# Kernel tuning notes

Measured on AMD Instinct MI355X. Metric: run time of the kernel, lower is better.

Reference implementation:

```python
import jax, jax.numpy as jnp
import numpy as np

D_MODEL = 1024
N_HEAD = 16
D_K = D_MODEL // N_HEAD
FF = 4096
EPS = 1e-5


def _linear(x, W, b):
    # torch nn.Linear: y = x @ W.T + b ; W stored [out, in]
    return jnp.einsum('bnd,od->bno', x, W) + b


def _mha(xq, xkv, Wq, bq, Wk, bk, Wv, bv):
    B, N, D = xq.shape
    M = xkv.shape[1]
    q = _linear(xq, Wq, bq).reshape(B, N, N_HEAD, D_K).transpose(0, 2, 1, 3)
    k = _linear(xkv, Wk, bk).reshape(B, M, N_HEAD, D_K).transpose(0, 2, 1, 3)
    v = _linear(xkv, Wv, bv).reshape(B, M, N_HEAD, D_K).transpose(0, 2, 1, 3)
    scores = jnp.einsum('bhnd,bhmd->bhnm', q, k) / np.sqrt(D_K).astype(np.float32)
    attn = jax.nn.softmax(scores, axis=-1)
    out = jnp.einsum('bhnm,bhmd->bhnd', attn, v)
    return out.transpose(0, 2, 1, 3).reshape(B, N, D)


def _layernorm(x, g, b):
    mu = jnp.mean(x, axis=-1, keepdims=True)
    var = jnp.mean((x - mu) ** 2, axis=-1, keepdims=True)
    return (x - mu) * jax.lax.rsqrt(var + EPS) * g + b


def setup_inputs() -> dict:
    key = jax.random.key(0)
    ks = jax.random.split(key, 24)
    s = 0.02
    d = {
        'x': jax.random.normal(ks[0], (8, 1024, D_MODEL), jnp.float32),
        'memory': jax.random.normal(ks[1], (8, 1024, D_MODEL), jnp.float32),
        'Wq1': jax.random.normal(ks[2], (D_MODEL, D_MODEL), jnp.float32) * s,
        'bq1': jnp.zeros((D_MODEL,), jnp.float32),
        'Wk1': jax.random.normal(ks[3], (D_MODEL, D_MODEL), jnp.float32) * s,
        'bk1': jnp.zeros((D_MODEL,), jnp.float32),
        'Wv1': jax.random.normal(ks[4], (D_MODEL, D_MODEL), jnp.float32) * s,
        'bv1': jnp.zeros((D_MODEL,), jnp.float32),
        'Wq2': jax.random.normal(ks[5], (D_MODEL, D_MODEL), jnp.float32) * s,
        'bq2': jnp.zeros((D_MODEL,), jnp.float32),
        'Wk2': jax.random.normal(ks[6], (D_MODEL, D_MODEL), jnp.float32) * s,
        'bk2': jnp.zeros((D_MODEL,), jnp.float32),
        'Wv2': jax.random.normal(ks[7], (D_MODEL, D_MODEL), jnp.float32) * s,
        'bv2': jnp.zeros((D_MODEL,), jnp.float32),
        'W1': jax.random.normal(ks[8], (FF, D_MODEL), jnp.float32) * s,
        'b1': jnp.zeros((FF,), jnp.float32),
        'W2': jax.random.normal(ks[9], (D_MODEL, FF), jnp.float32) * s,
        'b2': jnp.zeros((D_MODEL,), jnp.float32),
        'g1': jnp.ones((D_MODEL,), jnp.float32),
        'be1': jnp.zeros((D_MODEL,), jnp.float32),
        'g2': jnp.ones((D_MODEL,), jnp.float32),
        'be2': jnp.zeros((D_MODEL,), jnp.float32),
        'g3': jnp.ones((D_MODEL,), jnp.float32),
        'be3': jnp.zeros((D_MODEL,), jnp.float32),
    }
    return d


def reference(x, memory, Wq1, bq1, Wk1, bk1, Wv1, bv1,
              Wq2, bq2, Wk2, bk2, Wv2, bv2,
              W1, b1, W2, b2, g1, be1, g2, be2, g3, be3):
    # Post-LN decoder layer, eval mode (dropout = identity), no masks
    x = _layernorm(x + _mha(x, x, Wq1, bq1, Wk1, bk1, Wv1, bv1), g1, be1)
    x = _layernorm(x + _mha(x, memory, Wq2, bq2, Wk2, bk2, Wv2, bv2), g2, be2)
    h = jnp.einsum('hf,bnf->bnh', W2, jax.nn.relu(_linear(x, W1, b1))) + b2
    x = _layernorm(x + h, g3, be3)
    return x
```

## Files before the change

### kernel.cpp

```cpp
#include <hip/hip_runtime.h>
#include <hip/hip_bf16.h>

typedef __attribute__((ext_vector_type(8))) short bf16x8;
typedef __attribute__((ext_vector_type(4))) float f32x4;

#define DEVI static __device__ __forceinline__

constexpr int DM  = 1024;
constexpr int NH  = 16;
constexpr int FFD = 4096;
constexpr int BB  = 8;
constexpr int SEQ = 1024;
constexpr int TT  = BB * SEQ;

DEVI float bf2f(unsigned short u) {
    union { unsigned u32; float f; } v; v.u32 = ((unsigned)u) << 16; return v.f;
}
DEVI unsigned short f2bf(float f) {
    union { float f; unsigned u; } v; v.f = f;
    unsigned x = v.u;
    return (unsigned short)((x + 0x7fffu + ((x >> 16) & 1u)) >> 16);
}

DEVI void async_ld16(void* lds, const void* g) {
    __builtin_amdgcn_global_load_lds(
        (const __attribute__((address_space(1))) unsigned int*)g,
        (__attribute__((address_space(3))) unsigned int*)lds, 16, 0, 0);
}

__global__ __launch_bounds__(256) void k_cvt(const float* __restrict__ src,
                                             unsigned short* __restrict__ dst, int n) {
    int i = (blockIdx.x * 256 + threadIdx.x) * 4;
    if (i >= n) return;
    float4 v = *reinterpret_cast<const float4*>(src + i);
    ushort4 o;
    o.x = f2bf(v.x); o.y = f2bf(v.y); o.z = f2bf(v.z); o.w = f2bf(v.w);
    *reinterpret_cast<ushort4*>(dst + i) = o;
}

template <int ACT, int BIAS_ROW>
__global__ __launch_bounds__(256)
void k_gemm(const unsigned short* __restrict__ A,
            const unsigned short* __restrict__ W,
            const float* __restrict__ bias,
            unsigned short* __restrict__ C,
            int M, int N, int K) {
    __shared__ __align__(16) unsigned short As[128 * 32];
    __shared__ __align__(16) unsigned short Bs[128 * 32];
    const int tid  = threadIdx.x;
    const int lane = tid & 63, wave = tid >> 6;
    const int wm = wave & 1, wn = wave >> 1;
    const int l15 = lane & 15, quad = lane >> 4;
    const int m0 = blockIdx.y * 128;
    const int n0 = blockIdx.x * 128;

    f32x4 acc[4][4];
#pragma unroll
    for (int i = 0; i < 4; i++)
#pragma unroll
        for (int j = 0; j < 4; j++) acc[i][j] = (f32x4){0.f, 0.f, 0.f, 0.f};

    const int srow = lane >> 2;
    const int scol = (lane & 3) * 8;
    const unsigned short* Ag = A + (size_t)(m0 + wave * 32 + srow) * K + scol;
    const unsigned short* Wg = W + (size_t)(n0 + wave * 32 + srow) * K + scol;
    unsigned short* Al0 = As + (wave * 32) * 32;
    unsigned short* Al1 = As + (wave * 32 + 16) * 32;
    unsigned short* Bl0 = Bs + (wave * 32) * 32;
    unsigned short* Bl1 = Bs + (wave * 32 + 16) * 32;

    for (int kb = 0; kb < K; kb += 32) {
        __syncthreads();
        async_ld16(Al0, Ag + kb);
        async_ld16(Al1, Ag + (size_t)16 * K + kb);
        async_ld16(Bl0, Wg + kb);
        async_ld16(Bl1, Wg + (size_t)16 * K + kb);
        __syncthreads();
        bf16x8 af[4], bfv[4];
#pragma unroll
        for (int mt = 0; mt < 4; mt++)
            af[mt] = *(const bf16x8*)(As + (wm * 64 + mt * 16 + l15) * 32 + quad * 8);
#pragma unroll
        for (int nt = 0; nt < 4; nt++)
            bfv[nt] = *(const bf16x8*)(Bs + (wn * 64 + nt * 16 + l15) * 32 + quad * 8);
#pragma unroll
        for (int mt = 0; mt < 4; mt++)
#pragma unroll
            for (int nt = 0; nt < 4; nt++)
                acc[mt][nt] = __builtin_amdgcn_mfma_f32_16x16x32_bf16(af[mt], bfv[nt], acc[mt][nt], 0, 0, 0);
    }

#pragma unroll
    for (int mt = 0; mt < 4; mt++)
#pragma unroll
        for (int nt = 0; nt < 4; nt++) {
            const int col = n0 + wn * 64 + nt * 16 + l15;
            float bcol = BIAS_ROW ? 0.f : bias[col];
#pragma unroll
            for (int r = 0; r < 4; r++) {
                const int row = m0 + wm * 64 + mt * 16 + quad * 4 + r;
                float v = acc[mt][nt][r] + (BIAS_ROW ? bias[row] : bcol);
                if (ACT == 1) v = v > 0.f ? v : 0.f;
                C[(size_t)row * N + col] = f2bf(v);
            }
        }
}

__global__ __launch_bounds__(256)
void k_attn(const unsigned short* __restrict__ Q,
            const unsigned short* __restrict__ K,
            const unsigned short* __restrict__ Vt,
            unsigned short* __restrict__ O) {
    constexpr int LDP = 72;
    __shared__ __align__(16) unsigned short Ks[64 * 64];
    __shared__ __align__(16) unsigned short Vs[64 * 64];
    __shared__ __align__(16) unsigned short Ps[4][32 * LDP];
    const int tid  = threadIdx.x;
    const int lane = tid & 63, wave = tid >> 6;
    const int l15 = lane & 15, quad = lane >> 4;
    const int bh = blockIdx.y;
    const int b = bh >> 4, h = bh & 15;
    const int q0 = blockIdx.x * 128 + wave * 32;

    bf16x8 aq[2][2];
#pragma unroll
    for (int ntQ = 0; ntQ < 2; ntQ++)
#pragma unroll
        for (int kc = 0; kc < 2; kc++)
            aq[ntQ][kc] = *(const bf16x8*)(Q + (size_t)(b * SEQ + q0 + ntQ * 16 + l15) * DM
                                             + h * 64 + kc * 32 + quad * 8);

    f32x4 o_[4][2];
#pragma unroll
    for (int i = 0; i < 4; i++)
#pragma unroll
        for (int j = 0; j < 2; j++) o_[i][j] = (f32x4){0.f, 0.f, 0.f, 0.f};
    float m_[2] = {-1e30f, -1e30f}, l_[2] = {0.f, 0.f};

    const int srow  = lane >> 3;
    const int ctrue = (lane & 7) ^ srow;
    const int seg0 = wave, seg1 = wave + 4;
    const unsigned short* Kg = K  + (size_t)(b * SEQ) * DM + h * 64 + ctrue * 8;
    const unsigned short* Vg = Vt + (size_t)(h * 64) * TT + b * SEQ + ctrue * 8;

    for (int kt = 0; kt < SEQ; kt += 64) {
        __syncthreads();
        async_ld16(Ks + seg0 * 512, Kg + (size_t)(kt + seg0 * 8 + srow) * DM);
        async_ld16(Ks + seg1 * 512, Kg + (size_t)(kt + seg1 * 8 + srow) * DM);
        async_ld16(Vs + seg0 * 512, Vg + (size_t)(seg0 * 8 + srow) * TT + kt);
        async_ld16(Vs + seg1 * 512, Vg + (size_t)(seg1 * 8 + srow) * TT + kt);
        __syncthreads();

        f32x4 s[4][2];
#pragma unroll
        for (int i = 0; i < 4; i++)
#pragma unroll
            for (int j = 0; j < 2; j++) s[i][j] = (f32x4){0.f, 0.f, 0.f, 0.f};
#pragma unroll
        for (int kc = 0; kc < 2; kc++)
#pragma unroll
            for (int mtK = 0; mtK < 4; mtK++) {
                const int pos = (kc * 4 + quad) ^ (l15 & 7);
                bf16x8 kf = *(const bf16x8*)(Ks + (mtK * 16 + l15) * 64 + pos * 8);
#pragma unroll
                for (int ntQ = 0; ntQ < 2; ntQ++)
                    s[mtK][ntQ] = __builtin_amdgcn_mfma_f32_16x16x32_bf16(kf, aq[ntQ][kc], s[mtK][ntQ], 0, 0, 0);
            }

#pragma unroll
        for (int ntQ = 0; ntQ < 2; ntQ++) {
            float mx = -1e30f;
#pragma unroll
            for (int mtK = 0; mtK < 4; mtK++)
#pragma unroll
                for (int r = 0; r < 4; r++) mx = fmaxf(mx, s[mtK][ntQ][r]);
            mx = fmaxf(mx, __shfl_xor(mx, 16));
            mx = fmaxf(mx, __shfl_xor(mx, 32));
            const float mnew  = fmaxf(m_[ntQ], mx * 0.125f);
            const float alpha = __expf(m_[ntQ] - mnew);
            m_[ntQ] = mnew;
            float sum = 0.f;
#pragma unroll
            for (int mtK = 0; mtK < 4; mtK++) {
                float p0 = __expf(fmaf(s[mtK][ntQ][0], 0.125f, -mnew));
                float p1 = __expf(fmaf(s[mtK][ntQ][1], 0.125f, -mnew));
                float p2 = __expf(fmaf(s[mtK][ntQ][2], 0.125f, -mnew));
                float p3 = __expf(fmaf(s[mtK][ntQ][3], 0.125f, -mnew));
                sum += (p0 + p1) + (p2 + p3);
                ushort4 pk;
                pk.x = f2bf(p0); pk.y = f2bf(p1); pk.z = f2bf(p2); pk.w = f2bf(p3);
                *(ushort4*)(&Ps[wave][(ntQ * 16 + l15) * LDP + mtK * 16 + quad * 4]) = pk;
            }
            sum += __shfl_xor(sum, 16);
            sum += __shfl_xor(sum, 32);
            l_[ntQ] = l_[ntQ] * alpha + sum;
#pragma unroll
            for (int mtD = 0; mtD < 4; mtD++)
#pragma unroll
                for (int r = 0; r < 4; r++) o_[mtD][ntQ][r] *= alpha;
        }
        __asm__ volatile("s_waitcnt lgkmcnt(0)" ::: "memory");

        bf16x8 pf[2][2];
#pragma unroll
        for (int ntQ = 0; ntQ < 2; ntQ++)
#pragma unroll
            for (int kc2 = 0; kc2 < 2; kc2++)
                pf[ntQ][kc2] = *(const bf16x8*)(&Ps[wave][(ntQ * 16 + l15) * LDP + kc2 * 32 + quad * 8]);
#pragma unroll
        for (int kc2 = 0; kc2 < 2; kc2++)
#pragma unroll
            for (int mtD = 0; mtD < 4; mtD++) {
                const int pos = (kc2 * 4 + quad) ^ (l15 & 7);
                bf16x8 vf = *(const bf16x8*)(Vs + (mtD * 16 + l15) * 64 + pos * 8);
#pragma unroll
                for (int ntQ = 0; ntQ < 2; ntQ++)
                    o_[mtD][ntQ] = __builtin_amdgcn_mfma_f32_16x16x32_bf16(vf, pf[ntQ][kc2], o_[mtD][ntQ], 0, 0, 0);
            }
    }

#pragma unroll
    for (int ntQ = 0; ntQ < 2; ntQ++) {
        const float rl = 1.f / l_[ntQ];
        const size_t tok = (size_t)b * SEQ + q0 + ntQ * 16 + l15;
#pragma unroll
        for (int mtD = 0; mtD < 4; mtD++) {
            ushort4 ov;
            ov.x = f2bf(o_[mtD][ntQ][0] * rl);
            ov.y = f2bf(o_[mtD][ntQ][1] * rl);
            ov.z = f2bf(o_[mtD][ntQ][2] * rl);
            ov.w = f2bf(o_[mtD][ntQ][3] * rl);
            *(ushort4*)(O + tok * DM + h * 64 + mtD * 16 + quad * 4) = ov;
        }
    }
}

__global__ __launch_bounds__(256)
void k_add_ln(const unsigned short* __restrict__ Xa,
              const unsigned short* __restrict__ Xb,
              const float* __restrict__ g, const float* __restrict__ be,
              unsigned short* __restrict__ Y, float* __restrict__ Yf) {
    const int row = blockIdx.x;
    const int base = threadIdx.x * 4;
    const size_t off = (size_t)row * DM + base;
    ushort4 xa = *(const ushort4*)(Xa + off);
    ushort4 xb = *(const ushort4*)(Xb + off);
    float v[4];
    v[0] = bf2f(xa.x) + bf2f(xb.x);
    v[1] = bf2f(xa.y) + bf2f(xb.y);
    v[2] = bf2f(xa.z) + bf2f(xb.z);
    v[3] = bf2f(xa.w) + bf2f(xb.w);
    float s1 = v[0] + v[1] + v[2] + v[3];
    float s2 = v[0]*v[0] + v[1]*v[1] + v[2]*v[2] + v[3]*v[3];
#pragma unroll
    for (int o = 32; o; o >>= 1) { s1 += __shfl_xor(s1, o); s2 += __shfl_xor(s2, o); }
    __shared__ float rs1[4], rs2[4];
    if ((threadIdx.x & 63) == 0) { rs1[threadIdx.x >> 6] = s1; rs2[threadIdx.x >> 6] = s2; }
    __syncthreads();
    s1 = rs1[0] + rs1[1] + rs1[2] + rs1[3];
    s2 = rs2[0] + rs2[1] + rs2[2] + rs2[3];
    const float mu = s1 * (1.f / DM);
    const float var = s2 * (1.f / DM) - mu * mu;
    const float rstd = rsqrtf(var + 1e-5f);
    float y[4];
#pragma unroll
    for (int j = 0; j < 4; j++) y[j] = (v[j] - mu) * rstd * g[base + j] + be[base + j];
    if (Y) {
        ushort4 o;
        o.x = f2bf(y[0]); o.y = f2bf(y[1]); o.z = f2bf(y[2]); o.w = f2bf(y[3]);
        *(ushort4*)(Y + off) = o;
    }
    if (Yf) *(float4*)(Yf + off) = (float4){y[0], y[1], y[2], y[3]};
}

extern "C" void kernel_launch(void* const* d_in, const int* in_sizes, int n_in,
                              void* d_out, int out_size, void* d_ws, size_t ws_size,
                              hipStream_t stream) {
    const float* x    = (const float*)d_in[0];
    const float* mem  = (const float*)d_in[1];
    const float* Wq1  = (const float*)d_in[2];  const float* bq1 = (const float*)d_in[3];
    const float* Wk1  = (const float*)d_in[4];  const float* bk1 = (const float*)d_in[5];
    const float* Wv1  = (const float*)d_in[6];  const float* bv1 = (const float*)d_in[7];
    const float* Wq2  = (const float*)d_in[8];  const float* bq2 = (const float*)d_in[9];
    const float* Wk2  = (const float*)d_in[10]; const float* bk2 = (const float*)d_in[11];
    const float* Wv2  = (const float*)d_in[12]; const float* bv2 = (const float*)d_in[13];
    const float* W1   = (const float*)d_in[14]; const float* b1  = (const float*)d_in[15];
    const float* W2   = (const float*)d_in[16]; const float* b2  = (const float*)d_in[17];
    const float* g1   = (const float*)d_in[18]; const float* be1 = (const float*)d_in[19];
    const float* g2   = (const float*)d_in[20]; const float* be2 = (const float*)d_in[21];
    const float* g3   = (const float*)d_in[22]; const float* be3 = (const float*)d_in[23];
    float* out = (float*)d_out;

    const size_t MiB = 1u << 20;
    char* w = (char*)d_ws;
    unsigned short* Wq1b = (unsigned short*)(w + 0 * MiB);
    unsigned short* Wk1b = (unsigned short*)(w + 2 * MiB);
    unsigned short* Wv1b = (unsigned short*)(w + 4 * MiB);
    unsigned short* Wq2b = (unsigned short*)(w + 6 * MiB);
    unsigned short* Wk2b = (unsigned short*)(w + 8 * MiB);
    unsigned short* Wv2b = (unsigned short*)(w + 10 * MiB);
    unsigned short* W1b  = (unsigned short*)(w + 12 * MiB);
    unsigned short* W2b  = (unsigned short*)(w + 20 * MiB);
    unsigned short* xb   = (unsigned short*)(w + 28 * MiB);
    unsigned short* mb   = (unsigned short*)(w + 44 * MiB);
    unsigned short* Qb   = (unsigned short*)(w + 60 * MiB);
    unsigned short* Kb   = (unsigned short*)(w + 76 * MiB);
    unsigned short* Vtb  = (unsigned short*)(w + 92 * MiB);
    unsigned short* Ab   = (unsigned short*)(w + 108 * MiB);
    unsigned short* x1b  = (unsigned short*)(w + 124 * MiB);
    unsigned short* x2b  = (unsigned short*)(w + 140 * MiB);
    unsigned short* h1b  = (unsigned short*)(w + 60 * MiB);
    unsigned short* h2b  = (unsigned short*)(w + 124 * MiB);

    const dim3 blk(256);
    k_cvt<<<TT * DM / 1024, blk, 0, stream>>>(x,   xb,   TT * DM);
    k_cvt<<<TT * DM / 1024, blk, 0, stream>>>(mem, mb,   TT * DM);
    k_cvt<<<DM * DM / 1024, blk, 0, stream>>>(Wq1, Wq1b, DM * DM);
    k_cvt<<<DM * DM / 1024, blk, 0, stream>>>(Wk1, Wk1b, DM * DM);
    k_cvt<<<DM * DM / 1024, blk, 0, stream>>>(Wv1, Wv1b, DM * DM);
    k_cvt<<<DM * DM / 1024, blk, 0, stream>>>(Wq2, Wq2b, DM * DM);
    k_cvt<<<DM * DM / 1024, blk, 0, stream>>>(Wk2, Wk2b, DM * DM);
    k_cvt<<<DM * DM / 1024, blk, 0, stream>>>(Wv2, Wv2b, DM * DM);
    k_cvt<<<FFD * DM / 1024, blk, 0, stream>>>(W1, W1b, FFD * DM);
    k_cvt<<<FFD * DM / 1024, blk, 0, stream>>>(W2, W2b, FFD * DM);

    const dim3 gD(DM / 128, TT / 128);
    const dim3 gVt(TT / 128, DM / 128);
    const dim3 gF(FFD / 128, TT / 128);
    const dim3 gA(SEQ / 128, BB * NH);

    k_gemm<0,0><<<gD,  blk, 0, stream>>>(xb,   Wq1b, bq1, Qb,  TT, DM, DM);
    k_gemm<0,0><<<gD,  blk, 0, stream>>>(xb,   Wk1b, bk1, Kb,  TT, DM, DM);
    k_gemm<0,1><<<gVt, blk, 0, stream>>>(Wv1b, xb,   bv1, Vtb, DM, TT, DM);
    k_attn<<<gA, blk, 0, stream>>>(Qb, Kb, Vtb, Ab);
    k_add_ln<<<TT, blk, 0, stream>>>(xb, Ab, g1, be1, x1b, nullptr);
    k_gemm<0,0><<<gD,  blk, 0, stream>>>(x1b,  Wq2b, bq2, Qb,  TT, DM, DM);
    k_gemm<0,0><<<gD,  blk, 0, stream>>>(mb,   Wk2b, bk2, Kb,  TT, DM, DM);
    k_gemm<0,1><<<gVt, blk, 0, stream>>>(Wv2b, mb,   bv2, Vtb, DM, TT, DM);
    k_attn<<<gA, blk, 0, stream>>>(Qb, Kb, Vtb, Ab);
    k_add_ln<<<TT, blk, 0, stream>>>(x1b, Ab, g2, be2, x2b, nullptr);
    k_gemm<1,0><<<gF, blk, 0, stream>>>(x2b, W1b, b1, h1b, TT, FFD, DM);
    k_gemm<0,0><<<gD, blk, 0, stream>>>(h1b, W2b, b2, h2b, TT, DM, FFD);
    k_add_ln<<<TT, blk, 0, stream>>>(x2b, h2b, g3, be3, nullptr, out);
}
```

Measured before the change: 776.2 us.

## Fuse conversions into one launch, merge Q/K projection, add XCD-aware block swizzle

All ten fp32-to-bf16 conversions now run as a single kernel launch, which removes per-launch overhead. The self-attention Q and K projections are merged into one GEMM with N=2048 over the contiguous Wq1/Wk1 bf16 buffers. Attention takes row strides so it can read that interleaved QK output. GEMMs also gain a block-index swizzle that groups tiles per XCD so neighbouring tiles share L2, at the cost of extra index arithmetic and a wider output buffer.

```diff
diff --git a/kernel.cpp b/kernel.cpp
--- a/kernel.cpp
+++ b/kernel.cpp
@@ -28,31 +28,64 @@
         (__attribute__((address_space(3))) unsigned int*)lds, 16, 0, 0);
 }
 
-__global__ __launch_bounds__(256) void k_cvt(const float* __restrict__ src,
-                                             unsigned short* __restrict__ dst, int n) {
-    int i = (blockIdx.x * 256 + threadIdx.x) * 4;
-    if (i >= n) return;
-    float4 v = *reinterpret_cast<const float4*>(src + i);
+__global__ __launch_bounds__(256)
+void k_cvt_all(const float* __restrict__ s0, unsigned short* __restrict__ d0,
+               const float* __restrict__ s1, unsigned short* __restrict__ d1,
+               const float* __restrict__ s2, unsigned short* __restrict__ d2,
+               const float* __restrict__ s3, unsigned short* __restrict__ d3,
+               const float* __restrict__ s4, unsigned short* __restrict__ d4,
+               const float* __restrict__ s5, unsigned short* __restrict__ d5,
+               const float* __restrict__ s6, unsigned short* __restrict__ d6,
+               const float* __restrict__ s7, unsigned short* __restrict__ d7,
+               const float* __restrict__ s8, unsigned short* __restrict__ d8,
+               const float* __restrict__ s9, unsigned short* __restrict__ d9) {
+    int b = blockIdx.x;
+    const float* s; unsigned short* d;
+    if      (b < 8192)  { s = s0; d = d0; }
+    else if (b < 16384) { s = s1; d = d1; b -= 8192; }
+    else if (b < 17408) { s = s2; d = d2; b -= 16384; }
+    else if (b < 18432) { s = s3; d = d3; b -= 17408; }
+    else if (b < 19456) { s = s4; d = d4; b -= 18432; }
+    else if (b < 20480) { s = s5; d = d5; b -= 19456; }
+    else if (b < 21504) { s = s6; d = d6; b -= 20480; }
+    else if (b < 22528) { s = s7; d = d7; b -= 21504; }
+    else if (b < 26624) { s = s8; d = d8; b -= 22528; }
+    else                { s = s9; d = d9; b -= 26624; }
+    const int i = (b * 256 + threadIdx.x) * 4;
+    float4 v = *reinterpret_cast<const float4*>(s + i);
     ushort4 o;
     o.x = f2bf(v.x); o.y = f2bf(v.y); o.z = f2bf(v.z); o.w = f2bf(v.w);
-    *reinterpret_cast<ushort4*>(dst + i) = o;
-}
-
-template <int ACT, int BIAS_ROW>
+    *reinterpret_cast<ushort4*>(d + i) = o;
+}
+
+template <int ACT, int BIAS_ROW, int SWZ>
 __global__ __launch_bounds__(256)
 void k_gemm(const unsigned short* __restrict__ A,
             const unsigned short* __restrict__ W,
-            const float* __restrict__ bias,
+            const float* __restrict__ bias1, const float* __restrict__ bias2,
             unsigned short* __restrict__ C,
-            int M, int N, int K) {
+            int M, int N, int K, int Nsplit) {
     __shared__ __align__(16) unsigned short As[128 * 32];
     __shared__ __align__(16) unsigned short Bs[128 * 32];
     const int tid  = threadIdx.x;
     const int lane = tid & 63, wave = tid >> 6;
     const int wm = wave & 1, wn = wave >> 1;
     const int l15 = lane & 15, quad = lane >> 4;
-    const int m0 = blockIdx.y * 128;
-    const int n0 = blockIdx.x * 128;
+
+    int bx, by;
+    if (SWZ == 1) {
+        const int id = blockIdx.y * gridDim.x + blockIdx.x;
+        const int xcd = id & 7, i2 = id >> 3;
+        bx = i2 % gridDim.x;
+        by = (i2 / gridDim.x) * 8 + xcd;
+    } else if (SWZ == 2) {
+        const int id = blockIdx.y * gridDim.x + blockIdx.x;
+        const int xcd = id & 7, i2 = id >> 3;
+        by = i2 % gridDim.y;
+        bx = (i2 / gridDim.y) * 8 + xcd;
+    } else { bx = blockIdx.x; by = blockIdx.y; }
+    const int m0 = by * 128;
+    const int n0 = bx * 128;
 
     f32x4 acc[4][4];
 #pragma unroll
@@ -95,11 +128,12 @@
 #pragma unroll
         for (int nt = 0; nt < 4; nt++) {
             const int col = n0 + wn * 64 + nt * 16 + l15;
-            float bcol = BIAS_ROW ? 0.f : bias[col];
+            float bcol = 0.f;
+            if (!BIAS_ROW) bcol = col < Nsplit ? bias1[col] : bias2[col - Nsplit];
 #pragma unroll
             for (int r = 0; r < 4; r++) {
                 const int row = m0 + wm * 64 + mt * 16 + quad * 4 + r;
-                float v = acc[mt][nt][r] + (BIAS_ROW ? bias[row] : bcol);
+                float v = acc[mt][nt][r] + (BIAS_ROW ? bias1[row] : bcol);
                 if (ACT == 1) v = v > 0.f ? v : 0.f;
                 C[(size_t)row * N + col] = f2bf(v);
             }
@@ -110,7 +144,8 @@
 void k_attn(const unsigned short* __restrict__ Q,
             const unsigned short* __restrict__ K,
             const unsigned short* __restrict__ Vt,
-            unsigned short* __restrict__ O) {
+            unsigned short* __restrict__ O,
+            int qld, int kld) {
     constexpr int LDP = 72;
     __shared__ __align__(16) unsigned short Ks[64 * 64];
     __shared__ __align__(16) unsigned short Vs[64 * 64];
@@ -127,7 +162,7 @@
     for (int ntQ = 0; ntQ < 2; ntQ++)
 #pragma unroll
         for (int kc = 0; kc < 2; kc++)
-            aq[ntQ][kc] = *(const bf16x8*)(Q + (size_t)(b * SEQ + q0 + ntQ * 16 + l15) * DM
+            aq[ntQ][kc] = *(const bf16x8*)(Q + (size_t)(b * SEQ + q0 + ntQ * 16 + l15) * qld
                                              + h * 64 + kc * 32 + quad * 8);
 
     f32x4 o_[4][2];
@@ -140,13 +175,13 @@
     const int srow  = lane >> 3;
     const int ctrue = (lane & 7) ^ srow;
     const int seg0 = wave, seg1 = wave + 4;
-    const unsigned short* Kg = K  + (size_t)(b * SEQ) * DM + h * 64 + ctrue * 8;
+    const unsigned short* Kg = K  + (size_t)(b * SEQ) * kld + h * 64 + ctrue * 8;
     const unsigned short* Vg = Vt + (size_t)(h * 64) * TT + b * SEQ + ctrue * 8;
 
     for (int kt = 0; kt < SEQ; kt += 64) {
         __syncthreads();
-        async_ld16(Ks + seg0 * 512, Kg + (size_t)(kt + seg0 * 8 + srow) * DM);
-        async_ld16(Ks + seg1 * 512, Kg + (size_t)(kt + seg1 * 8 + srow) * DM);
+        async_ld16(Ks + seg0 * 512, Kg + (size_t)(kt + seg0 * 8 + srow) * kld);
+        async_ld16(Ks + seg1 * 512, Kg + (size_t)(kt + seg1 * 8 + srow) * kld);
         async_ld16(Vs + seg0 * 512, Vg + (size_t)(seg0 * 8 + srow) * TT + kt);
         async_ld16(Vs + seg1 * 512, Vg + (size_t)(seg1 * 8 + srow) * TT + kt);
         __syncthreads();
@@ -303,8 +338,9 @@
     unsigned short* W2b  = (unsigned short*)(w + 20 * MiB);
     unsigned short* xb   = (unsigned short*)(w + 28 * MiB);
     unsigned short* mb   = (unsigned short*)(w + 44 * MiB);
-    unsigned short* Qb   = (unsigned short*)(w + 60 * MiB);
-    unsigned short* Kb   = (unsigned short*)(w + 76 * MiB);
+    unsigned short* QKb  = (unsigned short*)(w + 60 * MiB);
+    unsigned short* Qb2  = (unsigned short*)(w + 60 * MiB);
+    unsigned short* Kb2  = (unsigned short*)(w + 76 * MiB);
     unsigned short* Vtb  = (unsigned short*)(w + 92 * MiB);
     unsigned short* Ab   = (unsigned short*)(w + 108 * MiB);
     unsigned short* x1b  = (unsigned short*)(w + 124 * MiB);
@@ -313,33 +349,26 @@
     unsigned short* h2b  = (unsigned short*)(w + 124 * MiB);
 
     const dim3 blk(256);
-    k_cvt<<<TT * DM / 1024, blk, 0, stream>>>(x,   xb,   TT * DM);
-    k_cvt<<<TT * DM / 1024, blk, 0, stream>>>(mem, mb,   TT * DM);
-    k_cvt<<<DM * DM / 1024, blk, 0, stream>>>(Wq1, Wq1b, DM * DM);
-    k_cvt<<<DM * DM / 1024, blk, 0, stream>>>(Wk1, Wk1b, DM * DM);
-    k_cvt<<<DM * DM / 1024, blk, 0, stream>>>(Wv1, Wv1b, DM * DM);
-    k_cvt<<<DM * DM / 1024, blk, 0, stream>>>(Wq2, Wq2b, DM * DM);
-    k_cvt<<<DM * DM / 1024, blk, 0, stream>>>(Wk2, Wk2b, DM * DM);
-    k_cvt<<<DM * DM / 1024, blk, 0, stream>>>(Wv2, Wv2b, DM * DM);
-    k_cvt<<<FFD * DM / 1024, blk, 0, stream>>>(W1, W1b, FFD * DM);
-    k_cvt<<<FFD * DM / 1024, blk, 0, stream>>>(W2, W2b, FFD * DM);
+    k_cvt_all<<<30720, blk, 0, stream>>>(x, xb, mem, mb, Wq1, Wq1b, Wk1, Wk1b,
+                                         Wv1, Wv1b, Wq2, Wq2b, Wk2, Wk2b,
+                                         Wv2, Wv2b, W1, W1b, W2, W2b);
 
     const dim3 gD(DM / 128, TT / 128);
+    const dim3 gQK(2048 / 128, TT / 128);
     const dim3 gVt(TT / 128, DM / 128);
     const dim3 gF(FFD / 128, TT / 128);
     const dim3 gA(SEQ / 128, BB * NH);
 
-    k_gemm<0,0><<<gD,  blk, 0, stream>>>(xb,   Wq1b, bq1, Qb,  TT, DM, DM);
-    k_gemm<0,0><<<gD,  blk, 0, stream>>>(xb,   Wk1b, bk1, Kb,  TT, DM, DM);
-    k_gemm<0,1><<<gVt, blk, 0, stream>>>(Wv1b, xb,   bv1, Vtb, DM, TT, DM);
-    k_attn<<<gA, blk, 0, stream>>>(Qb, Kb, Vtb, Ab);
+    k_gemm<0,0,1><<<gQK, blk, 0, stream>>>(xb,   Wq1b, bq1, bk1, QKb, TT, 2048, DM, 1024);
+    k_gemm<0,1,2><<<gVt, blk, 0, stream>>>(Wv1b, xb,   bv1, bv1, Vtb, DM, TT, DM, TT);
+    k_attn<<<gA, blk, 0, stream>>>(QKb, QKb + 1024, Vtb, Ab, 2048, 2048);
     k_add_ln<<<TT, blk, 0, stream>>>(xb, Ab, g1, be1, x1b, nullptr);
-    k_gemm<0,0><<<gD,  blk, 0, stream>>>(x1b,  Wq2b, bq2, Qb,  TT, DM, DM);
-    k_gemm<0,0><<<gD,  blk, 0, stream>>>(mb,   Wk2b, bk2, Kb,  TT, DM, DM);
-    k_gemm<0,1><<<gVt, blk, 0, stream>>>(Wv2b, mb,   bv2, Vtb, DM, TT, DM);
-    k_attn<<<gA, blk, 0, stream>>>(Qb, Kb, Vtb, Ab);
+    k_gemm<0,0,1><<<gD,  blk, 0, stream>>>(x1b,  Wq2b, bq2, bq2, Qb2, TT, DM, DM, DM);
+    k_gemm<0,0,1><<<gD,  blk, 0, stream>>>(mb,   Wk2b, bk2, bk2, Kb2, TT, DM, DM, DM);
+    k_gemm<0,1,2><<<gVt, blk, 0, stream>>>(Wv2b, mb,   bv2, bv2, Vtb, DM, TT, DM, TT);
+    k_attn<<<gA, blk, 0, stream>>>(Qb2, Kb2, Vtb, Ab, 1024, 1024);
     k_add_ln<<<TT, blk, 0, stream>>>(x1b, Ab, g2, be2, x2b, nullptr);
-    k_gemm<1,0><<<gF, blk, 0, stream>>>(x2b, W1b, b1, h1b, TT, FFD, DM);
-    k_gemm<0,0><<<gD, blk, 0, stream>>>(h1b, W2b, b2, h2b, TT, DM, FFD);
+    k_gemm<1,0,0><<<gF, blk, 0, stream>>>(x2b, W1b, b1, b1, h1b, TT, FFD, DM, FFD);
+    k_gemm<0,0,1><<<gD, blk, 0, stream>>>(h1b, W2b, b2, b2, h2b, TT, DM, FFD, DM);
     k_add_ln<<<TT, blk, 0, stream>>>(x2b, h2b, g3, be3, nullptr, out);
 }
```

Measured after the change: 733.2 us. 1.06x faster.
